# Optimization experiments

Measured on AMD Instinct MI355X. Metric: run time of the kernel, lower is better.

## Reference

```python
import jax, jax.numpy as jnp
import numpy as np

DIM = 768
NUM_HEADS = 12
HEAD_DIM = DIM // NUM_HEADS
SCALE = HEAD_DIM ** -0.5
NEG = -9e15


def setup_inputs() -> dict:
    key = jax.random.key(0)
    ks = jax.random.split(key, 8)
    B, N, M, C = 4, 1024, 2048, DIM
    q = jax.random.normal(ks[0], (B, N, C), dtype=jnp.float32)
    kv = jax.random.normal(ks[1], (B, M, C), dtype=jnp.float32)
    mask = jax.random.randint(ks[2], (B, 1, N, M), 0, 2, dtype=jnp.int32)
    s = 1.0 / np.sqrt(C)
    Wq = jax.random.normal(ks[3], (C, C), dtype=jnp.float32) * s      # nn.Linear(dim, dim), no bias
    Wkv = jax.random.normal(ks[4], (2 * C, C), dtype=jnp.float32) * s  # nn.Linear(dim, 2*dim), no bias
    Wproj = jax.random.normal(ks[5], (C, C), dtype=jnp.float32) * s
    bproj = jax.random.normal(ks[6], (C,), dtype=jnp.float32) * s
    return {"q": q, "kv": kv, "Wq": Wq, "Wkv": Wkv, "Wproj": Wproj, "bproj": bproj, "mask": mask}


def reference(q, kv, Wq, Wkv, Wproj, bproj, mask):
    B, M, C = kv.shape
    _, N, _ = q.shape
    H, d = NUM_HEADS, HEAD_DIM
    # kv projection -> [B, M, 2, H, d] -> k, v: [B, H, M, d]
    kvp = (kv @ Wkv.T).reshape(B, M, 2, H, d)
    k = kvp[:, :, 0].transpose(0, 2, 1, 3)
    v = kvp[:, :, 1].transpose(0, 2, 1, 3)
    # q projection -> [B, H, N, d], pre-scaled
    qp = (q @ Wq.T).reshape(B, N, H, d).transpose(0, 2, 1, 3) * SCALE
    attn = jnp.einsum('bhnd,bhmd->bhnm', qp, k)  # [B, H, N, M]
    attn = jnp.where(mask == 0, NEG, attn)
    attn = jax.nn.softmax(attn, axis=-1)
    # attn_drop / proj_drop have rate 0.0 (eval): identity
    x = jnp.einsum('bhnm,bhmd->bhnd', attn, v)
    x = x.transpose(0, 2, 1, 3).reshape(B, N, C)
    x = x @ Wproj.T + bproj
    return x
```

## Files before the change

kernel.cpp:

```cpp
#include <hip/hip_runtime.h>
#include <hip/hip_bf16.h>


typedef short    s16x8  __attribute__((ext_vector_type(8)));
typedef short    s16x4  __attribute__((ext_vector_type(4)));
typedef float    f32x4  __attribute__((ext_vector_type(4)));
typedef _Float16 f16x8  __attribute__((ext_vector_type(8)));
typedef _Float16 f16x4  __attribute__((ext_vector_type(4)));
typedef _Float16 f16x2  __attribute__((ext_vector_type(2)));

#define NUM_H 12
#define DIM   768
#define NQ    1024
#define MK    2048
#define QK_SCALE_LOG2E 0.18033688f

__device__ __forceinline__ short f2h(float v) {
    _Float16 h = (_Float16)v;
    return __builtin_bit_cast(short, h);
}
__device__ __forceinline__ f32x4 mfma16x32(f16x8 a, f16x8 b, f32x4 c) {
    return __builtin_amdgcn_mfma_f32_16x16x32_f16(a, b, c, 0, 0, 0);
}
__device__ __forceinline__ f16x2 pk2h(float a, float b) {
    return __builtin_bit_cast(f16x2, __builtin_amdgcn_cvt_pkrtz(a, b));
}

__global__ __launch_bounds__(256) void prep_kernel(
    const float* __restrict__ q, const float* __restrict__ kv,
    const float* __restrict__ Wq, const float* __restrict__ Wkv,
    const float* __restrict__ Wp, const int* __restrict__ mask,
    short* __restrict__ q_h, short* __restrict__ kv_h,
    short* __restrict__ Wq_h, short* __restrict__ Wkv_h,
    short* __restrict__ Wp_h, unsigned char* __restrict__ mbytes)
{
    int bid = blockIdx.x;
    if (bid < 5760) {
        const float* s; short* d; long base;
        if (bid < 1536)      { s = q;   d = q_h;   base = (long)bid * 2048; }
        else if (bid < 4608) { s = kv;  d = kv_h;  base = (long)(bid - 1536) * 2048; }
        else if (bid < 4896) { s = Wq;  d = Wq_h;  base = (long)(bid - 4608) * 2048; }
        else if (bid < 5472) { s = Wkv; d = Wkv_h; base = (long)(bid - 4896) * 2048; }
        else                 { s = Wp;  d = Wp_h;  base = (long)(bid - 5472) * 2048; }
        long i = base + threadIdx.x * 8;
        float4 a = *(const float4*)(s + i);
        float4 b = *(const float4*)(s + i + 4);
        s16x8 r;
        r[0] = f2h(a.x); r[1] = f2h(a.y); r[2] = f2h(a.z); r[3] = f2h(a.w);
        r[4] = f2h(b.x); r[5] = f2h(b.y); r[6] = f2h(b.z); r[7] = f2h(b.w);
        *(s16x8*)(d + i) = r;
    } else {
        long base = (long)(bid - 5760) * 2048 + threadIdx.x * 8;
        int4 m0 = *(const int4*)(mask + base);
        int4 m1 = *(const int4*)(mask + base + 4);
        unsigned v = (unsigned)(m0.x != 0)        | ((unsigned)(m0.y != 0) << 1)
                   | ((unsigned)(m0.z != 0) << 2) | ((unsigned)(m0.w != 0) << 3)
                   | ((unsigned)(m1.x != 0) << 4) | ((unsigned)(m1.y != 0) << 5)
                   | ((unsigned)(m1.z != 0) << 6) | ((unsigned)(m1.w != 0) << 7);
        mbytes[base >> 3] = (unsigned char)v;
    }
}

__device__ __forceinline__ void gemm_core(
    short* smem,
    const short* __restrict__ A, const short* __restrict__ Bt,
    int Ncols, int mode, const float* __restrict__ bias,
    short* __restrict__ outb, short* __restrict__ outb2,
    float* __restrict__ outf, int bid)
{
    short (*As)[72] = (short(*)[72])smem;
    short (*Bs)[72] = (short(*)[72])(smem + 9216);

    int ntiles = Ncols >> 7;
    int m0 = (bid / ntiles) << 7;
    int n0 = (bid % ntiles) << 7;
    int t = threadIdx.x;
    int w = t >> 6, lane = t & 63, quad = lane >> 4, l16 = lane & 15;
    int wm = (w & 1) << 6, wn = (w >> 1) << 6;

    f32x4 zero4 = {0.f, 0.f, 0.f, 0.f};
    f32x4 acc[4][4];
    for (int i = 0; i < 4; i++)
        for (int j = 0; j < 4; j++) acc[i][j] = zero4;

    int lr = t >> 1;
    int lc = (t & 1) << 5;
    const short* Ap = A + (long)(m0 + lr) * DIM + lc;
    const short* Bp = Bt + (long)(n0 + lr) * DIM + lc;

    s16x8 a0[4], b0[4], a1[4], b1[4];
    #pragma unroll
    for (int c = 0; c < 4; c++) {
        a0[c] = *(const s16x8*)(Ap + c * 8);
        b0[c] = *(const s16x8*)(Bp + c * 8);
        a1[c] = *(const s16x8*)(Ap + 64 + c * 8);
        b1[c] = *(const s16x8*)(Bp + 64 + c * 8);
    }

    auto mfma_tile = [&]() {
        #pragma unroll
        for (int kh = 0; kh < 2; kh++) {
            f16x8 af[4], bfr[4];
            #pragma unroll
            for (int i = 0; i < 4; i++)
                af[i] = __builtin_bit_cast(f16x8,
                    *(const s16x8*)&As[wm + i * 16 + l16][kh * 32 + quad * 8]);
            #pragma unroll
            for (int j = 0; j < 4; j++)
                bfr[j] = __builtin_bit_cast(f16x8,
                    *(const s16x8*)&Bs[wn + j * 16 + l16][kh * 32 + quad * 8]);
            #pragma unroll
            for (int i = 0; i < 4; i++)
                #pragma unroll
                for (int j = 0; j < 4; j++)
                    acc[i][j] = mfma16x32(af[i], bfr[j], acc[i][j]);
        }
    };

    for (int kt = 0; kt < DIM; kt += 128) {
        __syncthreads();
        #pragma unroll
        for (int c = 0; c < 4; c++) {
            *(s16x8*)&As[lr][lc + c * 8] = a0[c];
            *(s16x8*)&Bs[lr][lc + c * 8] = b0[c];
        }
        __syncthreads();
        if (kt + 128 < DIM) {
            #pragma unroll
            for (int c = 0; c < 4; c++) {
                a0[c] = *(const s16x8*)(Ap + kt + 128 + c * 8);
                b0[c] = *(const s16x8*)(Bp + kt + 128 + c * 8);
            }
        }
        mfma_tile();
        __syncthreads();
        #pragma unroll
        for (int c = 0; c < 4; c++) {
            *(s16x8*)&As[lr][lc + c * 8] = a1[c];
            *(s16x8*)&Bs[lr][lc + c * 8] = b1[c];
        }
        __syncthreads();
        if (kt + 192 < DIM) {
            #pragma unroll
            for (int c = 0; c < 4; c++) {
                a1[c] = *(const s16x8*)(Ap + kt + 192 + c * 8);
                b1[c] = *(const s16x8*)(Bp + kt + 192 + c * 8);
            }
        }
        mfma_tile();
    }

    __syncthreads();

    if (mode == 2) {
        #pragma unroll
        for (int i = 0; i < 4; i++)
            #pragma unroll
            for (int j = 0; j < 4; j++)
                #pragma unroll
                for (int r = 0; r < 4; r++) {
                    int row = m0 + wm + i * 16 + quad * 4 + r;
                    int col = n0 + wn + j * 16 + l16;
                    outf[(long)row * DIM + col] = acc[i][j][r] + bias[col];
                }
        return;
    }

    short (*Cs)[136] = (short(*)[136])smem;
    bool vreg = (mode == 1) && (n0 >= DIM);

    if (!vreg) {
        float sc = (mode == 0) ? QK_SCALE_LOG2E : 1.0f;
        #pragma unroll
        for (int i = 0; i < 4; i++)
            #pragma unroll
            for (int j = 0; j < 4; j++)
                #pragma unroll
                for (int r = 0; r < 4; r++)
                    Cs[wm + i * 16 + quad * 4 + r][wn + j * 16 + l16] =
                        f2h(acc[i][j][r] * sc);
    } else {
        #pragma unroll
        for (int i = 0; i < 4; i++)
            #pragma unroll
            for (int j = 0; j < 4; j++) {
                int c = wn + j * 16 + l16;
                int r0 = wm + i * 16 + quad * 4;
                s16x4 pk;
                pk[0] = f2h(acc[i][j][0]); pk[1] = f2h(acc[i][j][1]);
                pk[2] = f2h(acc[i][j][2]); pk[3] = f2h(acc[i][j][3]);
                *(s16x4*)&Cs[c][r0] = pk;
            }
    }
    __syncthreads();

    if (!vreg) {
        int hb2 = n0 >> 6;
        long rowsN = (mode == 0) ? NQ : MK;
        int b = (int)(m0 / rowsN);
        int rb = (int)(m0 % rowsN);
        short* ob0 = outb + ((long)(b * NUM_H + hb2) * rowsN + rb) * 64;
        short* ob1 = outb + ((long)(b * NUM_H + hb2 + 1) * rowsN + rb) * 64;
        #pragma unroll
        for (int k2 = 0; k2 < 8; k2++) {
            int ch = k2 * 256 + t;
            int half = ch >> 10, off = ch & 1023;
            s16x8 vd = *(const s16x8*)&Cs[off >> 3][(half << 6) + ((off & 7) << 3)];
            *(s16x8*)((half ? ob1 : ob0) + off * 8) = vd;
        }
    } else {
        int hb2 = (n0 - DIM) >> 6;
        int b = m0 >> 11, rb = m0 & 2047;
        #pragma unroll
        for (int k2 = 0; k2 < 8; k2++) {
            int ch = k2 * 256 + t;
            int c = ch >> 4, woff = (ch & 15) << 3;
            s16x8 vd = *(const s16x8*)&Cs[c][woff];
            int half = c >> 6, dd = c & 63;
            *(s16x8*)(outb2 + (((long)(b * NUM_H + hb2 + half) * 64 + dd) * MK + rb) + woff) = vd;
        }
    }
}

__global__ __launch_bounds__(256) void gemm12_kernel(
    const short* __restrict__ qh, const short* __restrict__ Wqh,
    const short* __restrict__ kvh, const short* __restrict__ Wkvh,
    short* __restrict__ qp, short* __restrict__ kk, short* __restrict__ vt)
{
    __shared__ short smem[18432];
    if (blockIdx.x < 192)
        gemm_core(smem, qh, Wqh, 768, 0, nullptr, qp, nullptr, nullptr, blockIdx.x);
    else
        gemm_core(smem, kvh, Wkvh, 1536, 1, nullptr, kk, vt, nullptr, blockIdx.x - 192);
}

__global__ __launch_bounds__(256) void gemm3_kernel(
    const short* __restrict__ xb, const short* __restrict__ Wph,
    const float* __restrict__ bias, float* __restrict__ out)
{
    __shared__ short smem[18432];
    gemm_core(smem, xb, Wph, 768, 2, bias, nullptr, nullptr, out, blockIdx.x);
}

__global__ __launch_bounds__(256) void attn_kernel(
    const short* __restrict__ qp, const short* __restrict__ kk,
    const short* __restrict__ vt, const unsigned* __restrict__ mb,
    short* __restrict__ xb)
{
    __shared__ short qs[128][72];
    __shared__ short ks[64][72];
    __shared__ short vs[64][72];

    int bid = blockIdx.x;
    int bh = bid % 48;
    int nt = bid / 48;
    int h = bh % NUM_H, b = bh / NUM_H;
    int n0 = nt << 7;
    int t = threadIdx.x, w = t >> 6, lane = t & 63, quad = lane >> 4, l16 = lane & 15;

    const short* qbase = qp + ((long)bh * NQ + n0) * 64;
    const short* kbase = kk + (long)bh * MK * 64;
    const short* vbase = vt + (long)bh * 64 * MK;
    const unsigned* mrow0 = mb + ((long)b * NQ + n0 + (w << 5) + l16) * 64;
    const unsigned* mrow1 = mrow0 + 16 * 64;

    {
        int qr = t >> 1, c0 = (t & 1) << 5;
        #pragma unroll
        for (int c = 0; c < 4; c++)
            *(s16x8*)&qs[qr][c0 + c * 8] = *(const s16x8*)(qbase + qr * 64 + c0 + c * 8);
    }
    __syncthreads();
    f16x8 bq[2][2];
    #pragma unroll
    for (int s2 = 0; s2 < 2; s2++)
        #pragma unroll
        for (int kh = 0; kh < 2; kh++)
            bq[s2][kh] = __builtin_bit_cast(f16x8,
                *(const s16x8*)&qs[(w << 5) + (s2 << 4) + l16][kh * 32 + quad * 8]);

    int sr = t >> 2, c0 = (t & 3) << 4;
    int pr = (sr & 32) + ((sr & 4) << 2) + ((sr & 24) >> 1) + (sr & 3);
    const short* kp = kbase + (long)sr * 64 + c0;
    const short* vp = vbase + (long)sr * MK + c0;

    s16x8 k0 = *(const s16x8*)(kp);
    s16x8 k1 = *(const s16x8*)(kp + 8);
    s16x8 v0 = *(const s16x8*)(vp);
    s16x8 v1 = *(const s16x8*)(vp + 8);
    uint2 mwv0 = *(const uint2*)(mrow0);
    uint2 mwv1 = *(const uint2*)(mrow1);

    f32x4 zero4 = {0.f, 0.f, 0.f, 0.f};
    f32x4 o[2][4], ol[2];
    #pragma unroll
    for (int s2 = 0; s2 < 2; s2++) {
        ol[s2] = zero4;
        for (int j = 0; j < 4; j++) o[s2][j] = zero4;
    }
    const f16x8 ones = {(_Float16)1.f, (_Float16)1.f, (_Float16)1.f, (_Float16)1.f,
                        (_Float16)1.f, (_Float16)1.f, (_Float16)1.f, (_Float16)1.f};

    for (int mt = 0; mt < MK; mt += 64) {
        __syncthreads();
        *(s16x8*)&ks[pr][c0]     = k0;
        *(s16x8*)&ks[pr][c0 + 8] = k1;
        *(s16x8*)&vs[sr][c0]     = v0;
        *(s16x8*)&vs[sr][c0 + 8] = v1;
        unsigned cm[2][2] = {{mwv0.x, mwv0.y}, {mwv1.x, mwv1.y}};
        __syncthreads();
        if (mt + 64 < MK) {
            k0 = *(const s16x8*)(kp + (long)(mt + 64) * 64);
            k1 = *(const s16x8*)(kp + (long)(mt + 64) * 64 + 8);
            v0 = *(const s16x8*)(vp + mt + 64);
            v1 = *(const s16x8*)(vp + mt + 64 + 8);
            mwv0 = *(const uint2*)(mrow0 + ((mt + 64) >> 5));
            mwv1 = *(const uint2*)(mrow1 + ((mt + 64) >> 5));
        }

        f32x4 s[2][4];
        #pragma unroll
        for (int jj = 0; jj < 4; jj++) { s[0][jj] = zero4; s[1][jj] = zero4; }
        #pragma unroll
        for (int kh = 0; kh < 2; kh++)
            #pragma unroll
            for (int jj = 0; jj < 4; jj++) {
                f16x8 ak = __builtin_bit_cast(f16x8,
                    *(const s16x8*)&ks[jj * 16 + l16][kh * 32 + quad * 8]);
                s[0][jj] = mfma16x32(ak, bq[0][kh], s[0][jj]);
                s[1][jj] = mfma16x32(ak, bq[1][kh], s[1][jj]);
            }

        f16x8 pa[2][2];
        #pragma unroll
        for (int s2 = 0; s2 < 2; s2++)
            #pragma unroll
            for (int j2 = 0; j2 < 2; j2++) {
                unsigned wsel = cm[s2][j2];
                f16x2 pk[4];
                #pragma unroll
                for (int sub = 0; sub < 2; sub++) {
                    unsigned bits = wsel >> ((quad << 3) + (sub << 2));
                    const f32x4& sv = s[s2][j2 * 2 + sub];
                    float p0 = (bits & 1u)        ? __builtin_amdgcn_exp2f(sv[0]) : 0.f;
                    float p1 = ((bits >> 1) & 1u) ? __builtin_amdgcn_exp2f(sv[1]) : 0.f;
                    float p2 = ((bits >> 2) & 1u) ? __builtin_amdgcn_exp2f(sv[2]) : 0.f;
                    float p3 = ((bits >> 3) & 1u) ? __builtin_amdgcn_exp2f(sv[3]) : 0.f;
                    pk[sub * 2]     = pk2h(p0, p1);
                    pk[sub * 2 + 1] = pk2h(p2, p3);
                }
                f16x4 lo = __builtin_shufflevector(pk[0], pk[1], 0, 1, 2, 3);
                f16x4 hi = __builtin_shufflevector(pk[2], pk[3], 0, 1, 2, 3);
                pa[s2][j2] = __builtin_shufflevector(lo, hi, 0, 1, 2, 3, 4, 5, 6, 7);
            }

        #pragma unroll
        for (int j2 = 0; j2 < 2; j2++) {
            ol[0] = mfma16x32(pa[0][j2], ones, ol[0]);
            ol[1] = mfma16x32(pa[1][j2], ones, ol[1]);
            #pragma unroll
            for (int jd = 0; jd < 4; jd++) {
                f16x8 bv = __builtin_bit_cast(f16x8,
                    *(const s16x8*)&vs[jd * 16 + l16][j2 * 32 + quad * 8]);
                o[0][jd] = mfma16x32(pa[0][j2], bv, o[0][jd]);
                o[1][jd] = mfma16x32(pa[1][j2], bv, o[1][jd]);
            }
        }
    }

    __syncthreads();
    #pragma unroll
    for (int s2 = 0; s2 < 2; s2++) {
        float linv[4];
        #pragma unroll
        for (int rr = 0; rr < 4; rr++) linv[rr] = 1.0f / ol[s2][rr];
        #pragma unroll
        for (int jd = 0; jd < 4; jd++)
            #pragma unroll
            for (int rr = 0; rr < 4; rr++)
                qs[(w << 5) + (s2 << 4) + quad * 4 + rr][jd * 16 + l16] =
                    f2h(o[s2][jd][rr] * linv[rr]);
    }
    #pragma unroll
    for (int k2 = 0; k2 < 4; k2++) {
        int row = (w << 5) + (lane >> 3) + k2 * 8;
        int cc = (lane & 7) << 3;
        s16x8 vd = *(const s16x8*)&qs[row][cc];
        *(s16x8*)(xb + ((long)b * NQ + n0 + row) * DIM + h * 64 + cc) = vd;
    }
}

extern "C" void kernel_launch(void* const* d_in, const int* in_sizes, int n_in,
                              void* d_out, int out_size, void* d_ws, size_t ws_size,
                              hipStream_t stream)
{
    const float* q     = (const float*)d_in[0];
    const float* kv    = (const float*)d_in[1];
    const float* Wq    = (const float*)d_in[2];
    const float* Wkv   = (const float*)d_in[3];
    const float* Wproj = (const float*)d_in[4];
    const float* bproj = (const float*)d_in[5];
    const int*   mask  = (const int*)d_in[6];
    float* out = (float*)d_out;

    char* ws = (char*)d_ws;
    short* q_h   = (short*)ws; ws += (size_t)4096 * 768 * 2;
    short* kv_h  = (short*)ws; ws += (size_t)8192 * 768 * 2;
    short* Wq_h  = (short*)ws; ws += (size_t)768 * 768 * 2;
    short* Wkv_h = (short*)ws; ws += (size_t)1536 * 768 * 2;
    short* Wp_h  = (short*)ws; ws += (size_t)768 * 768 * 2;
    short* qp    = (short*)ws; ws += (size_t)4096 * 768 * 2;
    short* kk    = (short*)ws; ws += (size_t)8192 * 768 * 2;
    short* vt    = (short*)ws; ws += (size_t)8192 * 768 * 2;
    short* xb    = (short*)ws; ws += (size_t)4096 * 768 * 2;
    unsigned char* mbytes = (unsigned char*)ws;

    prep_kernel<<<9856, 256, 0, stream>>>(q, kv, Wq, Wkv, Wproj, mask,
                                          q_h, kv_h, Wq_h, Wkv_h, Wp_h, mbytes);
    gemm12_kernel<<<960, 256, 0, stream>>>(q_h, Wq_h, kv_h, Wkv_h, qp, kk, vt);
    attn_kernel<<<384, 256, 0, stream>>>(qp, kk, vt, (const unsigned*)mbytes, xb);
    gemm3_kernel<<<192, 256, 0, stream>>>(xb, Wp_h, bproj, out);
}
```

Baseline: 223.0 us.

## Split attention over key dimension into two halves with a combine kernel

Result: faster. 214.9 us (-3.6%).

```diff
diff --git a/kernel.cpp b/kernel.cpp
--- a/kernel.cpp
+++ b/kernel.cpp
@@ -18,6 +18,9 @@
 __device__ __forceinline__ short f2h(float v) {
     _Float16 h = (_Float16)v;
     return __builtin_bit_cast(short, h);
+}
+__device__ __forceinline__ float h2f(short v) {
+    return (float)__builtin_bit_cast(_Float16, v);
 }
 __device__ __forceinline__ f32x4 mfma16x32(f16x8 a, f16x8 b, f32x4 c) {
     return __builtin_amdgcn_mfma_f32_16x16x32_f16(a, b, c, 0, 0, 0);
@@ -56,7 +59,8 @@
         unsigned v = (unsigned)(m0.x != 0)        | ((unsigned)(m0.y != 0) << 1)
                    | ((unsigned)(m0.z != 0) << 2) | ((unsigned)(m0.w != 0) << 3)
                    | ((unsigned)(m1.x != 0) << 4) | ((unsigned)(m1.y != 0) << 5)
-                   | ((unsigned)(m1.z != 0) << 6) | ((unsigned)(m1.w != 0) << 7);
+                   | ((unsigned)(m1.z != 0) << 6) | ((unsigned)(m1.w << 7) & 0x80);
+        v = (v & 0x7f) | ((unsigned)(m1.w != 0) << 7);
         mbytes[base >> 3] = (unsigned char)v;
     }
 }
@@ -245,7 +249,7 @@
 __global__ __launch_bounds__(256) void attn_kernel(
     const short* __restrict__ qp, const short* __restrict__ kk,
     const short* __restrict__ vt, const unsigned* __restrict__ mb,
-    short* __restrict__ xb)
+    short* __restrict__ po, float* __restrict__ pl)
 {
     __shared__ short qs[128][72];
     __shared__ short ks[64][72];
@@ -253,22 +257,23 @@
 
     int bid = blockIdx.x;
     int bh = bid % 48;
-    int nt = bid / 48;
+    int rest = bid / 48;
+    int mhalf = rest & 1, nt = rest >> 1;
     int h = bh % NUM_H, b = bh / NUM_H;
     int n0 = nt << 7;
     int t = threadIdx.x, w = t >> 6, lane = t & 63, quad = lane >> 4, l16 = lane & 15;
 
     const short* qbase = qp + ((long)bh * NQ + n0) * 64;
-    const short* kbase = kk + (long)bh * MK * 64;
-    const short* vbase = vt + (long)bh * 64 * MK;
-    const unsigned* mrow0 = mb + ((long)b * NQ + n0 + (w << 5) + l16) * 64;
+    const short* kbase = kk + (long)bh * MK * 64 + (long)mhalf * 1024 * 64;
+    const short* vbase = vt + (long)bh * 64 * MK + mhalf * 1024;
+    const unsigned* mrow0 = mb + ((long)b * NQ + n0 + (w << 5) + l16) * 64 + (mhalf << 5);
     const unsigned* mrow1 = mrow0 + 16 * 64;
 
     {
-        int qr = t >> 1, c0 = (t & 1) << 5;
+        int qr = t >> 1, c0q = (t & 1) << 5;
         #pragma unroll
         for (int c = 0; c < 4; c++)
-            *(s16x8*)&qs[qr][c0 + c * 8] = *(const s16x8*)(qbase + qr * 64 + c0 + c * 8);
+            *(s16x8*)&qs[qr][c0q + c * 8] = *(const s16x8*)(qbase + qr * 64 + c0q + c * 8);
     }
     __syncthreads();
     f16x8 bq[2][2];
@@ -301,7 +306,7 @@
     const f16x8 ones = {(_Float16)1.f, (_Float16)1.f, (_Float16)1.f, (_Float16)1.f,
                         (_Float16)1.f, (_Float16)1.f, (_Float16)1.f, (_Float16)1.f};
 
-    for (int mt = 0; mt < MK; mt += 64) {
+    for (int mt = 0; mt < 1024; mt += 64) {
         __syncthreads();
         *(s16x8*)&ks[pr][c0]     = k0;
         *(s16x8*)&ks[pr][c0 + 8] = k1;
@@ -309,7 +314,7 @@
         *(s16x8*)&vs[sr][c0 + 8] = v1;
         unsigned cm[2][2] = {{mwv0.x, mwv0.y}, {mwv1.x, mwv1.y}};
         __syncthreads();
-        if (mt + 64 < MK) {
+        if (mt + 64 < 1024) {
             k0 = *(const s16x8*)(kp + (long)(mt + 64) * 64);
             k1 = *(const s16x8*)(kp + (long)(mt + 64) * 64 + 8);
             v0 = *(const s16x8*)(vp + mt + 64);
@@ -368,26 +373,52 @@
         }
     }
 
+    long slot = (long)(mhalf * 384 + bh * 8 + nt);
     __syncthreads();
     #pragma unroll
     for (int s2 = 0; s2 < 2; s2++) {
-        float linv[4];
-        #pragma unroll
-        for (int rr = 0; rr < 4; rr++) linv[rr] = 1.0f / ol[s2][rr];
         #pragma unroll
         for (int jd = 0; jd < 4; jd++)
             #pragma unroll
             for (int rr = 0; rr < 4; rr++)
                 qs[(w << 5) + (s2 << 4) + quad * 4 + rr][jd * 16 + l16] =
-                    f2h(o[s2][jd][rr] * linv[rr]);
-    }
+                    f2h(o[s2][jd][rr]);
+        if (l16 == 0) {
+            #pragma unroll
+            for (int rr = 0; rr < 4; rr++)
+                pl[slot * 128 + (w << 5) + (s2 << 4) + quad * 4 + rr] = ol[s2][rr];
+        }
+    }
+    __syncthreads();
+    short* pbase = po + slot * 128 * 64;
     #pragma unroll
     for (int k2 = 0; k2 < 4; k2++) {
-        int row = (w << 5) + (lane >> 3) + k2 * 8;
-        int cc = (lane & 7) << 3;
-        s16x8 vd = *(const s16x8*)&qs[row][cc];
-        *(s16x8*)(xb + ((long)b * NQ + n0 + row) * DIM + h * 64 + cc) = vd;
-    }
+        int ch = k2 * 256 + t;
+        int row = ch >> 3, cc = (ch & 7) << 3;
+        *(s16x8*)(pbase + row * 64 + cc) = *(const s16x8*)&qs[row][cc];
+    }
+}
+
+__global__ __launch_bounds__(256) void combine_kernel(
+    const short* __restrict__ po, const float* __restrict__ pl,
+    short* __restrict__ xb)
+{
+    int g = blockIdx.x * 256 + threadIdx.x;
+    int rs = g >> 3, c8 = (g & 7) << 3;
+    int bh = rs >> 10, rem = rs & 1023;
+    int nt = rem >> 7, r = rem & 127;
+    int b = bh / NUM_H, h = bh % NUM_H;
+    int n = (nt << 7) + r;
+
+    float l = pl[rs] + pl[49152 + rs];
+    float linv = 1.0f / l;
+    s16x8 x0 = *(const s16x8*)(po + (long)rs * 64 + c8);
+    s16x8 x1 = *(const s16x8*)(po + (long)(49152 + rs) * 64 + c8);
+    s16x8 r8;
+    #pragma unroll
+    for (int i = 0; i < 8; i++)
+        r8[i] = f2h((h2f(x0[i]) + h2f(x1[i])) * linv);
+    *(s16x8*)(xb + ((long)(b * NQ) + n) * DIM + h * 64 + c8) = r8;
 }
 
 extern "C" void kernel_launch(void* const* d_in, const int* in_sizes, int n_in,
@@ -413,11 +444,14 @@
     short* kk    = (short*)ws; ws += (size_t)8192 * 768 * 2;
     short* vt    = (short*)ws; ws += (size_t)8192 * 768 * 2;
     short* xb    = (short*)ws; ws += (size_t)4096 * 768 * 2;
-    unsigned char* mbytes = (unsigned char*)ws;
+    unsigned char* mbytes = (unsigned char*)ws; ws += (size_t)1 << 20;
+    short* po    = (short*)ws; ws += (size_t)2 * 49152 * 64 * 2;
+    float* pl    = (float*)ws;
 
     prep_kernel<<<9856, 256, 0, stream>>>(q, kv, Wq, Wkv, Wproj, mask,
                                           q_h, kv_h, Wq_h, Wkv_h, Wp_h, mbytes);
     gemm12_kernel<<<960, 256, 0, stream>>>(q_h, Wq_h, kv_h, Wkv_h, qp, kk, vt);
-    attn_kernel<<<384, 256, 0, stream>>>(qp, kk, vt, (const unsigned*)mbytes, xb);
+    attn_kernel<<<768, 256, 0, stream>>>(qp, kk, vt, (const unsigned*)mbytes, po, pl);
+    combine_kernel<<<1536, 256, 0, stream>>>(po, pl, xb);
     gemm3_kernel<<<192, 256, 0, stream>>>(xb, Wp_h, bproj, out);
 }
```
